# Kernel optimization log

Measured on AMD Instinct MI355X. Metric: run time of the kernel, lower is better.

## Reference

```python
import jax, jax.numpy as jnp
import numpy as np

N = 100000   # num nodes
D = 64       # in_channels == out_channels (forced by zeros_like(x) accumulator)
E = 400000   # edges per edge type
T = 5        # number of edge types (hardcoded list in the module)


def setup_inputs() -> dict:
    key = jax.random.key(0)
    k1, k2, k3, k4, k5 = jax.random.split(key, 5)
    x = jax.random.normal(k1, (N, D), dtype=jnp.float32)
    # 5 edge types, each [2, E] of node indices (row 0 = src, row 1 = dst)
    edges = jax.random.randint(k2, (T, 2, E), 0, N)
    # per-edge-type Linear(2D -> D): weight [2D, D] and bias [D]
    W = jax.random.normal(k3, (T, 2 * D, D), dtype=jnp.float32) * (1.0 / np.sqrt(2 * D))
    b = jax.random.normal(k4, (T, D), dtype=jnp.float32) * 0.01
    edge_attention = jax.random.normal(k5, (T,), dtype=jnp.float32)
    return {"x": x, "W": W, "b": b, "edge_attention": edge_attention, "edges": edges}


def reference(x, W, b, edge_attention, edges):
    # softmax over the 5 edge types (F.softmax(self.edge_attention, dim=0))
    weights = jax.nn.softmax(edge_attention)              # [T]
    src = edges[:, 0, :]                                  # [T, E]
    dst = edges[:, 1, :]                                  # [T, E]
    # gather: edge_features = cat([x[src], x[dst]], dim=1)
    feats = jnp.concatenate([x[src], x[dst]], axis=-1)    # [T, E, 2D]
    # per-edge-type MLP: Linear(2D->D) + ReLU
    proj = jax.nn.relu(jnp.einsum('tef,tfd->ted', feats, W) + b[:, None, :])  # [T, E, D]
    # scatter-add into src nodes, then mean via clamped bincount
    seg_sum = jax.vmap(lambda s, p: jax.ops.segment_sum(p, s, num_segments=N))(src, proj)  # [T, N, D]
    counts = jax.vmap(lambda s: jax.ops.segment_sum(jnp.ones(s.shape, jnp.float32), s, num_segments=N))(src)  # [T, N]
    counts = jnp.maximum(counts, 1.0)[:, :, None]         # clamp(min=1)
    node_proj = seg_sum / counts                          # [T, N, D]
    # attention-weighted sum across edge types
    return jnp.einsum('t,tnd->nd', weights, node_proj)    # [N, D]
```

## Files before the change

### kernel.cpp

```cpp
#include <hip/hip_runtime.h>
#include <hip/hip_bf16.h>

#define NN 100000
#define DD 64
#define EE 400000
#define TT 5

#define CH 40
#define BPC 2500
#define PSPLIT 32
#define PESL (EE / PSPLIT)
#define PBN (TT * CH * PSPLIT)
#define PB_IDX(t, c, s) ((((t) * CH + (c)) * PSPLIT) + (s))

typedef __bf16 bf16x8 __attribute__((ext_vector_type(8)));
typedef float  f32x4  __attribute__((ext_vector_type(4)));

#define OFF_XBF  0u
#define OFF_WT   12800000u
#define OFF_CTOT 12881920u
#define OFF_WGT  14881920u
#define OFF_PE   16886080u
#define OFF_PB   24886080u
#define OFF_DST  24914240u
#define OFF_SEG  32914240u

__device__ __forceinline__ unsigned short f2bf(float f) {
    union { float f; unsigned u; } v; v.f = f;
    unsigned u = v.u;
    return (unsigned short)((u + 0x7FFFu + ((u >> 16) & 1u)) >> 16);
}

__global__ __launch_bounds__(256) void k_init(
        const float* __restrict__ x, const float* __restrict__ W,
        const float* __restrict__ ea, const int* __restrict__ edges,
        unsigned short* __restrict__ xbf, unsigned short* __restrict__ wT,
        float* __restrict__ wgt, float* __restrict__ out,
        unsigned* __restrict__ pcnt) {
    int i = blockIdx.x * blockDim.x + threadIdx.x;
    if (i < NN * DD) {
        out[i] = 0.0f;
        xbf[i] = f2bf(x[i]);
    }
    if (i < TT * 128 * 64) {
        int t = i >> 13;
        int rem = i & 8191;
        int d = rem >> 7;
        int k = rem & 127;
        wT[i] = f2bf(W[t * 8192 + k * 64 + d]);
    }
    if (i == 0) {
        float m = -1e30f;
        for (int t = 0; t < TT; t++) m = fmaxf(m, ea[t]);
        float e[TT]; float s = 0.0f;
        for (int t = 0; t < TT; t++) { e[t] = __expf(ea[t] - m); s += e[t]; }
        for (int t = 0; t < TT; t++) wgt[t] = e[t] / s;
    }
    if (blockIdx.x < PSPLIT * TT) {
        const int s = blockIdx.x & (PSPLIT - 1);
        const int t = blockIdx.x >> 5;
        __shared__ unsigned h[CH];
        if (threadIdx.x < CH) h[threadIdx.x] = 0u;
        __syncthreads();
        const int4* srcp = reinterpret_cast<const int4*>(edges + (size_t)t * 2 * EE + s * PESL);
        for (int j = threadIdx.x; j < PESL / 4; j += 256) {
            int4 v = srcp[j];
            atomicAdd(&h[(unsigned)v.x / BPC], 1u);
            atomicAdd(&h[(unsigned)v.y / BPC], 1u);
            atomicAdd(&h[(unsigned)v.z / BPC], 1u);
            atomicAdd(&h[(unsigned)v.w / BPC], 1u);
        }
        __syncthreads();
        if (threadIdx.x < CH) pcnt[PB_IDX(t, threadIdx.x, s)] = h[threadIdx.x];
    }
}

__global__ __launch_bounds__(256) void k_pscat(const int* __restrict__ edges,
                                               const unsigned* __restrict__ pb,
                                               unsigned* __restrict__ pe) {
    const int s = blockIdx.x, t = blockIdx.y;
    const int tid = threadIdx.x;
    __shared__ unsigned pbs[PBN];
    __shared__ unsigned ssum[256];
    __shared__ unsigned lofs[CH];
    {
        const int base = tid * 25;
        unsigned v[25]; unsigned sum = 0u;
#pragma unroll
        for (int j = 0; j < 25; j++) { v[j] = pb[base + j]; sum += v[j]; }
        ssum[tid] = sum;
        __syncthreads();
        unsigned inc = sum;
        for (int d = 1; d < 256; d <<= 1) {
            unsigned a = (tid >= d) ? ssum[tid - d] : 0u;
            __syncthreads();
            inc += a;
            ssum[tid] = inc;
            __syncthreads();
        }
        unsigned run = inc - sum;
#pragma unroll
        for (int j = 0; j < 25; j++) { pbs[base + j] = run; run += v[j]; }
        __syncthreads();
        if (tid < CH) lofs[tid] = pbs[PB_IDX(t, tid, s)];
        __syncthreads();
    }
    const int* srcp = edges + (size_t)t * 2 * EE + s * PESL;
    const int* dstp = srcp + EE;
    for (int i = tid; i < PESL / 4; i += 256) {
        int4 v = reinterpret_cast<const int4*>(srcp)[i];
        int4 w = reinterpret_cast<const int4*>(dstp)[i];
        {
            unsigned c = (unsigned)v.x / BPC;
            unsigned o = atomicAdd(&lofs[c], 1u);
            pe[o] = (((unsigned)v.x - c * BPC) << 17) | (unsigned)w.x;
        }
        {
            unsigned c = (unsigned)v.y / BPC;
            unsigned o = atomicAdd(&lofs[c], 1u);
            pe[o] = (((unsigned)v.y - c * BPC) << 17) | (unsigned)w.y;
        }
        {
            unsigned c = (unsigned)v.z / BPC;
            unsigned o = atomicAdd(&lofs[c], 1u);
            pe[o] = (((unsigned)v.z - c * BPC) << 17) | (unsigned)w.z;
        }
        {
            unsigned c = (unsigned)v.w / BPC;
            unsigned o = atomicAdd(&lofs[c], 1u);
            pe[o] = (((unsigned)v.w - c * BPC) << 17) | (unsigned)w.w;
        }
    }
}

__global__ __launch_bounds__(512) void k_bsort(const unsigned* __restrict__ pe,
                                               const unsigned* __restrict__ pb,
                                               unsigned* __restrict__ cnt_tot,
                                               int* __restrict__ sdst,
                                               int* __restrict__ seg) {
    const int c = blockIdx.x, t = blockIdx.y;
    const int tid = threadIdx.x;
    __shared__ unsigned h[BPC];
    __shared__ unsigned curl[BPC];
    __shared__ unsigned ssum[512];
    __shared__ unsigned stsh[2];

    const int K = (t * CH + c) * PSPLIT;

    unsigned part = 0u;
    for (int i = tid; i < K; i += 512) part += pb[i];
    ssum[tid] = part;
    __syncthreads();
    for (int d = 256; d > 0; d >>= 1) {
        if (tid < d) ssum[tid] += ssum[tid + d];
        __syncthreads();
    }
    if (tid == 0) stsh[0] = ssum[0];
    unsigned part2 = (tid < PSPLIT) ? pb[K + tid] : 0u;
    __syncthreads();
    ssum[tid] = part2;
    __syncthreads();
    for (int d = 256; d > 0; d >>= 1) {
        if (tid < d) ssum[tid] += ssum[tid + d];
        __syncthreads();
    }
    if (tid == 0) stsh[1] = ssum[0];
    for (int i = tid; i < BPC; i += 512) h[i] = 0u;
    __syncthreads();
    const unsigned st = stsh[0];
    const unsigned en = st + stsh[1];

    for (unsigned i = st + tid; i < en; i += 512)
        atomicAdd(&h[pe[i] >> 17], 1u);
    __syncthreads();

    unsigned* outp = cnt_tot + t * NN + c * BPC;
    for (int i = tid; i < BPC; i += 512) outp[i] = h[i];

    {
        const int base = tid * 5;
        unsigned v[5]; unsigned sum = 0u;
#pragma unroll
        for (int j = 0; j < 5; j++) {
            int g = base + j;
            v[j] = (g < BPC) ? h[g] : 0u;
            sum += v[j];
        }
        ssum[tid] = sum;
        __syncthreads();
        unsigned inc = sum;
        for (int d = 1; d < 512; d <<= 1) {
            unsigned a = (tid >= d) ? ssum[tid - d] : 0u;
            __syncthreads();
            inc += a;
            ssum[tid] = inc;
            __syncthreads();
        }
        unsigned run = st + inc - sum;
#pragma unroll
        for (int j = 0; j < 5; j++) {
            int g = base + j;
            if (g < BPC) {
                curl[g] = run;
                const int node = c * BPC + g;
                for (unsigned jj = 0; jj < v[j]; jj++) seg[run + jj] = node;
                run += v[j];
            }
        }
    }
    __syncthreads();

    for (unsigned i = st + tid; i < en; i += 512) {
        unsigned p = pe[i];
        sdst[atomicAdd(&curl[p >> 17], 1u)] = (int)(p & 0x1FFFFu);
    }
}

__global__ __launch_bounds__(256) void k_edge(
    const unsigned short* __restrict__ xbf, const unsigned short* __restrict__ wT,
    const float* __restrict__ b, const int* __restrict__ sdst,
    const int* __restrict__ seg, const unsigned* __restrict__ cnt,
    const float* __restrict__ wgt, float* __restrict__ out) {
    const int t  = blockIdx.y;
    const int e0 = blockIdx.x * 128;

    __shared__ __align__(16) unsigned short Ab[128][136];
    __shared__ float scale_s[128];
    __shared__ int   src_s[132];

    const int tid = threadIdx.x;

    {
        int e = tid >> 1, half = tid & 1;
        size_t pos = (size_t)t * EE + e0 + e;
        int idx = half ? sdst[pos] : seg[pos];
        const float4* g = reinterpret_cast<const float4*>(xbf + (size_t)idx * 64);
        float4* l = reinterpret_cast<float4*>(&Ab[e][half * 64]);
#pragma unroll
        for (int c = 0; c < 8; c++) l[c] = g[c];
        if (half == 0) {
            src_s[e] = idx;
            scale_s[e] = wgt[t] / (float)cnt[t * NN + idx];
        }
    }
    __syncthreads();

    const int wv = tid >> 6, lane = tid & 63;
    const int m16 = lane & 15, quad = lane >> 4;
    const unsigned short* wrow = wT + (size_t)t * 8192;

    f32x4 acc[2][4];
#pragma unroll
    for (int tm = 0; tm < 2; tm++)
#pragma unroll
        for (int tn = 0; tn < 4; tn++)
            acc[tm][tn] = (f32x4){0.f, 0.f, 0.f, 0.f};

#pragma unroll
    for (int kk = 0; kk < 128; kk += 32) {
        const int kb = kk + quad * 8;
        bf16x8 af[2], bfr[4];
#pragma unroll
        for (int tm = 0; tm < 2; tm++)
            af[tm] = *reinterpret_cast<const bf16x8*>(&Ab[wv * 32 + tm * 16 + m16][kb]);
#pragma unroll
        for (int tn = 0; tn < 4; tn++)
            bfr[tn] = *reinterpret_cast<const bf16x8*>(wrow + (tn * 16 + m16) * 128 + kb);
#pragma unroll
        for (int tm = 0; tm < 2; tm++)
#pragma unroll
            for (int tn = 0; tn < 4; tn++)
                acc[tm][tn] = __builtin_amdgcn_mfma_f32_16x16x32_bf16(
                    af[tm], bfr[tn], acc[tm][tn], 0, 0, 0);
    }

    __syncthreads();

    float bias[4];
#pragma unroll
    for (int tn = 0; tn < 4; tn++) bias[tn] = b[t * 64 + tn * 16 + m16];

    float* proj = reinterpret_cast<float*>(&Ab[0][0]);
#pragma unroll
    for (int tm = 0; tm < 2; tm++) {
#pragma unroll
        for (int r = 0; r < 4; r++) {
            const int eloc = wv * 32 + tm * 16 + quad * 4 + r;
            const float s = scale_s[eloc];
#pragma unroll
            for (int tn = 0; tn < 4; tn++) {
                float v = acc[tm][tn][r] + bias[tn];
                v = v > 0.f ? v : 0.f;
                proj[eloc * 68 + tn * 16 + m16] = v * s;
            }
        }
    }

    {
        const int j0 = wv * 32;
        float sum = 0.f;
#pragma unroll
        for (int j = j0; j < j0 + 32; j++) {
            sum += proj[j * 68 + lane];
            const bool flush = (j == j0 + 31) || (src_s[j + 1] != src_s[j]);
            if (flush) {
                atomicAdd(out + (size_t)src_s[j] * 64 + lane, sum);
                sum = 0.f;
            }
        }
    }
}

extern "C" void kernel_launch(void* const* d_in, const int* in_sizes, int n_in,
                              void* d_out, int out_size, void* d_ws, size_t ws_size,
                              hipStream_t stream) {
    const float* x     = (const float*)d_in[0];
    const float* W     = (const float*)d_in[1];
    const float* b     = (const float*)d_in[2];
    const float* ea    = (const float*)d_in[3];
    const int*   edges = (const int*)d_in[4];
    float* out = (float*)d_out;

    char* ws = (char*)d_ws;
    unsigned short* xbf  = (unsigned short*)(ws + OFF_XBF);
    unsigned short* wT   = (unsigned short*)(ws + OFF_WT);
    unsigned* cnt_tot    = (unsigned*)(ws + OFF_CTOT);
    float* wgt           = (float*)(ws + OFF_WGT);
    unsigned* pe         = (unsigned*)(ws + OFF_PE);
    unsigned* pb         = (unsigned*)(ws + OFF_PB);
    int* sdst            = (int*)(ws + OFF_DST);
    int* seg             = (int*)(ws + OFF_SEG);

    k_init<<<(NN * DD) / 256, 256, 0, stream>>>(x, W, ea, edges, xbf, wT, wgt, out, pb);

    k_pscat<<<dim3(PSPLIT, TT), 256, 0, stream>>>(edges, pb, pe);

    k_bsort<<<dim3(CH, TT), 512, 0, stream>>>(pe, pb, cnt_tot, sdst, seg);

    dim3 grid(EE / 128, TT);
    k_edge<<<grid, 256, 0, stream>>>(xbf, wT, b, sdst, seg, cnt_tot, wgt, out);
}
```

Before: 317.4 us.

## Merge edge types into one global sort by source node, mask per-type GEMM

```diff
diff --git a/kernel.cpp b/kernel.cpp
--- a/kernel.cpp
+++ b/kernel.cpp
@@ -6,12 +6,14 @@
 #define EE 400000
 #define TT 5
 
-#define CH 40
-#define BPC 2500
+#define CH 160
+#define BPC 625
 #define PSPLIT 32
 #define PESL (EE / PSPLIT)
-#define PBN (TT * CH * PSPLIT)
-#define PB_IDX(t, c, s) ((((t) * CH + (c)) * PSPLIT) + (s))
+#define NSB (PSPLIT * TT)
+#define PBN (CH * NSB)
+#define NBIN (BPC * TT)
+#define NETOT (TT * EE)
 
 typedef __bf16 bf16x8 __attribute__((ext_vector_type(8)));
 typedef float  f32x4  __attribute__((ext_vector_type(4)));
@@ -20,8 +22,8 @@
 #define OFF_WT   12800000u
 #define OFF_CTOT 12881920u
 #define OFF_WGT  14881920u
+#define OFF_PB   14882048u
 #define OFF_PE   16886080u
-#define OFF_PB   24886080u
 #define OFF_DST  24914240u
 #define OFF_SEG  32914240u
 
@@ -56,9 +58,10 @@
         for (int t = 0; t < TT; t++) { e[t] = __expf(ea[t] - m); s += e[t]; }
         for (int t = 0; t < TT; t++) wgt[t] = e[t] / s;
     }
-    if (blockIdx.x < PSPLIT * TT) {
-        const int s = blockIdx.x & (PSPLIT - 1);
-        const int t = blockIdx.x >> 5;
+    if (blockIdx.x < NSB) {
+        const int sb = blockIdx.x;
+        const int s = sb & (PSPLIT - 1);
+        const int t = sb >> 5;
         __shared__ unsigned h[CH];
         if (threadIdx.x < CH) h[threadIdx.x] = 0u;
         __syncthreads();
@@ -71,64 +74,64 @@
             atomicAdd(&h[(unsigned)v.w / BPC], 1u);
         }
         __syncthreads();
-        if (threadIdx.x < CH) pcnt[PB_IDX(t, threadIdx.x, s)] = h[threadIdx.x];
-    }
+        if (threadIdx.x < CH) pcnt[threadIdx.x * NSB + sb] = h[threadIdx.x];
+    }
+}
+
+__global__ void k_pscan(unsigned* __restrict__ pb) {
+    __shared__ unsigned s[1024];
+    const int tid = threadIdx.x;
+    unsigned v[25]; unsigned sum = 0u;
+#pragma unroll
+    for (int j = 0; j < 25; j++) { v[j] = pb[tid * 25 + j]; sum += v[j]; }
+    s[tid] = sum;
+    __syncthreads();
+    unsigned inc = sum;
+    for (int d = 1; d < 1024; d <<= 1) {
+        unsigned a = (tid >= d) ? s[tid - d] : 0u;
+        __syncthreads();
+        inc += a;
+        s[tid] = inc;
+        __syncthreads();
+    }
+    unsigned run = inc - sum;
+#pragma unroll
+    for (int j = 0; j < 25; j++) { unsigned c = v[j]; pb[tid * 25 + j] = run; run += c; }
 }
 
 __global__ __launch_bounds__(256) void k_pscat(const int* __restrict__ edges,
-                                               const unsigned* __restrict__ pb,
+                                               const unsigned* __restrict__ pbase,
                                                unsigned* __restrict__ pe) {
     const int s = blockIdx.x, t = blockIdx.y;
-    const int tid = threadIdx.x;
-    __shared__ unsigned pbs[PBN];
-    __shared__ unsigned ssum[256];
+    const int sb = t * PSPLIT + s;
     __shared__ unsigned lofs[CH];
-    {
-        const int base = tid * 25;
-        unsigned v[25]; unsigned sum = 0u;
-#pragma unroll
-        for (int j = 0; j < 25; j++) { v[j] = pb[base + j]; sum += v[j]; }
-        ssum[tid] = sum;
-        __syncthreads();
-        unsigned inc = sum;
-        for (int d = 1; d < 256; d <<= 1) {
-            unsigned a = (tid >= d) ? ssum[tid - d] : 0u;
-            __syncthreads();
-            inc += a;
-            ssum[tid] = inc;
-            __syncthreads();
-        }
-        unsigned run = inc - sum;
-#pragma unroll
-        for (int j = 0; j < 25; j++) { pbs[base + j] = run; run += v[j]; }
-        __syncthreads();
-        if (tid < CH) lofs[tid] = pbs[PB_IDX(t, tid, s)];
-        __syncthreads();
-    }
+    if (threadIdx.x < CH) lofs[threadIdx.x] = pbase[threadIdx.x * NSB + sb];
+    __syncthreads();
     const int* srcp = edges + (size_t)t * 2 * EE + s * PESL;
     const int* dstp = srcp + EE;
-    for (int i = tid; i < PESL / 4; i += 256) {
+    const unsigned tb = (unsigned)t << 17;
+    for (int i = threadIdx.x; i < PESL / 4; i += 256) {
         int4 v = reinterpret_cast<const int4*>(srcp)[i];
         int4 w = reinterpret_cast<const int4*>(dstp)[i];
         {
             unsigned c = (unsigned)v.x / BPC;
             unsigned o = atomicAdd(&lofs[c], 1u);
-            pe[o] = (((unsigned)v.x - c * BPC) << 17) | (unsigned)w.x;
+            pe[o] = (((unsigned)v.x - c * BPC) << 20) | tb | (unsigned)w.x;
         }
         {
             unsigned c = (unsigned)v.y / BPC;
             unsigned o = atomicAdd(&lofs[c], 1u);
-            pe[o] = (((unsigned)v.y - c * BPC) << 17) | (unsigned)w.y;
+            pe[o] = (((unsigned)v.y - c * BPC) << 20) | tb | (unsigned)w.y;
         }
         {
             unsigned c = (unsigned)v.z / BPC;
             unsigned o = atomicAdd(&lofs[c], 1u);
-            pe[o] = (((unsigned)v.z - c * BPC) << 17) | (unsigned)w.z;
+            pe[o] = (((unsigned)v.z - c * BPC) << 20) | tb | (unsigned)w.z;
         }
         {
             unsigned c = (unsigned)v.w / BPC;
             unsigned o = atomicAdd(&lofs[c], 1u);
-            pe[o] = (((unsigned)v.w - c * BPC) << 17) | (unsigned)w.w;
+            pe[o] = (((unsigned)v.w - c * BPC) << 20) | tb | (unsigned)w.w;
         }
     }
 }
@@ -138,52 +141,36 @@
                                                unsigned* __restrict__ cnt_tot,
                                                int* __restrict__ sdst,
                                                int* __restrict__ seg) {
-    const int c = blockIdx.x, t = blockIdx.y;
+    const int c = blockIdx.x;
     const int tid = threadIdx.x;
-    __shared__ unsigned h[BPC];
-    __shared__ unsigned curl[BPC];
+    __shared__ unsigned h[NBIN];
+    __shared__ unsigned curl[NBIN];
     __shared__ unsigned ssum[512];
-    __shared__ unsigned stsh[2];
-
-    const int K = (t * CH + c) * PSPLIT;
-
-    unsigned part = 0u;
-    for (int i = tid; i < K; i += 512) part += pb[i];
-    ssum[tid] = part;
-    __syncthreads();
-    for (int d = 256; d > 0; d >>= 1) {
-        if (tid < d) ssum[tid] += ssum[tid + d];
-        __syncthreads();
-    }
-    if (tid == 0) stsh[0] = ssum[0];
-    unsigned part2 = (tid < PSPLIT) ? pb[K + tid] : 0u;
-    __syncthreads();
-    ssum[tid] = part2;
-    __syncthreads();
-    for (int d = 256; d > 0; d >>= 1) {
-        if (tid < d) ssum[tid] += ssum[tid + d];
-        __syncthreads();
-    }
-    if (tid == 0) stsh[1] = ssum[0];
-    for (int i = tid; i < BPC; i += 512) h[i] = 0u;
-    __syncthreads();
-    const unsigned st = stsh[0];
-    const unsigned en = st + stsh[1];
-
-    for (unsigned i = st + tid; i < en; i += 512)
-        atomicAdd(&h[pe[i] >> 17], 1u);
-    __syncthreads();
-
-    unsigned* outp = cnt_tot + t * NN + c * BPC;
-    for (int i = tid; i < BPC; i += 512) outp[i] = h[i];
+
+    const unsigned st = pb[c * NSB];
+    const unsigned en = (c == CH - 1) ? (unsigned)NETOT : pb[(c + 1) * NSB];
+
+    for (int i = tid; i < NBIN; i += 512) h[i] = 0u;
+    __syncthreads();
+
+    for (unsigned i = st + tid; i < en; i += 512) {
+        unsigned p = pe[i];
+        atomicAdd(&h[(p >> 20) * TT + ((p >> 17) & 7u)], 1u);
+    }
+    __syncthreads();
+
+    for (int g = tid; g < NBIN; g += 512) {
+        int sl = g / TT, t = g - sl * TT;
+        cnt_tot[t * NN + c * BPC + sl] = h[g];
+    }
 
     {
-        const int base = tid * 5;
-        unsigned v[5]; unsigned sum = 0u;
-#pragma unroll
-        for (int j = 0; j < 5; j++) {
+        const int base = tid * 7;
+        unsigned v[7]; unsigned sum = 0u;
+#pragma unroll
+        for (int j = 0; j < 7; j++) {
             int g = base + j;
-            v[j] = (g < BPC) ? h[g] : 0u;
+            v[j] = (g < NBIN) ? h[g] : 0u;
             sum += v[j];
         }
         ssum[tid] = sum;
@@ -198,12 +185,13 @@
         }
         unsigned run = st + inc - sum;
 #pragma unroll
-        for (int j = 0; j < 5; j++) {
+        for (int j = 0; j < 7; j++) {
             int g = base + j;
-            if (g < BPC) {
+            if (g < NBIN) {
                 curl[g] = run;
-                const int node = c * BPC + g;
-                for (unsigned jj = 0; jj < v[j]; jj++) seg[run + jj] = node;
+                int sl = g / TT, t = g - sl * TT;
+                int val = ((c * BPC + sl) << 3) | t;
+                for (unsigned jj = 0; jj < v[j]; jj++) seg[run + jj] = val;
                 run += v[j];
             }
         }
@@ -212,42 +200,54 @@
 
     for (unsigned i = st + tid; i < en; i += 512) {
         unsigned p = pe[i];
-        sdst[atomicAdd(&curl[p >> 17], 1u)] = (int)(p & 0x1FFFFu);
-    }
-}
-
-__global__ __launch_bounds__(256) void k_edge(
+        unsigned bin = (p >> 20) * TT + ((p >> 17) & 7u);
+        sdst[atomicAdd(&curl[bin], 1u)] = (int)(p & 0x1FFFFu);
+    }
+}
+
+__global__ __launch_bounds__(256) void k_edge7(
     const unsigned short* __restrict__ xbf, const unsigned short* __restrict__ wT,
     const float* __restrict__ b, const int* __restrict__ sdst,
     const int* __restrict__ seg, const unsigned* __restrict__ cnt,
     const float* __restrict__ wgt, float* __restrict__ out) {
-    const int t  = blockIdx.y;
     const int e0 = blockIdx.x * 128;
 
     __shared__ __align__(16) unsigned short Ab[128][136];
     __shared__ float scale_s[128];
     __shared__ int   src_s[132];
+    __shared__ int   t_s[132];
+    __shared__ float bs[TT * 64];
 
     const int tid = threadIdx.x;
 
     {
         int e = tid >> 1, half = tid & 1;
-        size_t pos = (size_t)t * EE + e0 + e;
-        int idx = half ? sdst[pos] : seg[pos];
+        int pos = e0 + e;
+        int sv = seg[pos];
+        int srcI = sv >> 3, tE = sv & 7;
+        int idx = half ? sdst[pos] : srcI;
         const float4* g = reinterpret_cast<const float4*>(xbf + (size_t)idx * 64);
         float4* l = reinterpret_cast<float4*>(&Ab[e][half * 64]);
 #pragma unroll
         for (int c = 0; c < 8; c++) l[c] = g[c];
         if (half == 0) {
-            src_s[e] = idx;
-            scale_s[e] = wgt[t] / (float)cnt[t * NN + idx];
-        }
-    }
+            src_s[e] = srcI;
+            t_s[e] = tE;
+            scale_s[e] = wgt[tE] / (float)cnt[tE * NN + srcI];
+        }
+    }
+    for (int i = tid; i < TT * 64; i += 256) bs[i] = b[i];
     __syncthreads();
 
     const int wv = tid >> 6, lane = tid & 63;
     const int m16 = lane & 15, quad = lane >> 4;
-    const unsigned short* wrow = wT + (size_t)t * 8192;
+
+    const int tA0 = t_s[wv * 32 + m16];
+    const int tA1 = t_s[wv * 32 + 16 + m16];
+
+    bf16x8 z;
+#pragma unroll
+    for (int i = 0; i < 8; i++) z[i] = (__bf16)0.0f;
 
     f32x4 acc[2][4];
 #pragma unroll
@@ -257,28 +257,29 @@
             acc[tm][tn] = (f32x4){0.f, 0.f, 0.f, 0.f};
 
 #pragma unroll
-    for (int kk = 0; kk < 128; kk += 32) {
-        const int kb = kk + quad * 8;
-        bf16x8 af[2], bfr[4];
-#pragma unroll
-        for (int tm = 0; tm < 2; tm++)
-            af[tm] = *reinterpret_cast<const bf16x8*>(&Ab[wv * 32 + tm * 16 + m16][kb]);
-#pragma unroll
-        for (int tn = 0; tn < 4; tn++)
-            bfr[tn] = *reinterpret_cast<const bf16x8*>(wrow + (tn * 16 + m16) * 128 + kb);
-#pragma unroll
-        for (int tm = 0; tm < 2; tm++)
+    for (int p = 0; p < TT; p++) {
+        const unsigned short* wrow = wT + (size_t)p * 8192;
+        const bool m0 = (tA0 == p), m1 = (tA1 == p);
+#pragma unroll
+        for (int kk = 0; kk < 128; kk += 32) {
+            const int kb = kk + quad * 8;
+            bf16x8 a0 = *reinterpret_cast<const bf16x8*>(&Ab[wv * 32 + m16][kb]);
+            bf16x8 a1 = *reinterpret_cast<const bf16x8*>(&Ab[wv * 32 + 16 + m16][kb]);
+            a0 = m0 ? a0 : z;
+            a1 = m1 ? a1 : z;
+            bf16x8 bfr[4];
 #pragma unroll
             for (int tn = 0; tn < 4; tn++)
-                acc[tm][tn] = __builtin_amdgcn_mfma_f32_16x16x32_bf16(
-                    af[tm], bfr[tn], acc[tm][tn], 0, 0, 0);
-    }
-
-    __syncthreads();
-
-    float bias[4];
-#pragma unroll
-    for (int tn = 0; tn < 4; tn++) bias[tn] = b[t * 64 + tn * 16 + m16];
+                bfr[tn] = *reinterpret_cast<const bf16x8*>(wrow + (tn * 16 + m16) * 128 + kb);
+#pragma unroll
+            for (int tn = 0; tn < 4; tn++) {
+                acc[0][tn] = __builtin_amdgcn_mfma_f32_16x16x32_bf16(a0, bfr[tn], acc[0][tn], 0, 0, 0);
+                acc[1][tn] = __builtin_amdgcn_mfma_f32_16x16x32_bf16(a1, bfr[tn], acc[1][tn], 0, 0, 0);
+            }
+        }
+    }
+
+    __syncthreads();
 
     float* proj = reinterpret_cast<float*>(&Ab[0][0]);
 #pragma unroll
@@ -287,9 +288,10 @@
         for (int r = 0; r < 4; r++) {
             const int eloc = wv * 32 + tm * 16 + quad * 4 + r;
             const float s = scale_s[eloc];
+            const int tE = t_s[eloc];
 #pragma unroll
             for (int tn = 0; tn < 4; tn++) {
-                float v = acc[tm][tn][r] + bias[tn];
+                float v = acc[tm][tn][r] + bs[tE * 64 + tn * 16 + m16];
                 v = v > 0.f ? v : 0.f;
                 proj[eloc * 68 + tn * 16 + m16] = v * s;
             }
@@ -333,10 +335,11 @@
 
     k_init<<<(NN * DD) / 256, 256, 0, stream>>>(x, W, ea, edges, xbf, wT, wgt, out, pb);
 
+    k_pscan<<<1, 1024, 0, stream>>>(pb);
+
     k_pscat<<<dim3(PSPLIT, TT), 256, 0, stream>>>(edges, pb, pe);
 
-    k_bsort<<<dim3(CH, TT), 512, 0, stream>>>(pe, pb, cnt_tot, sdst, seg);
-
-    dim3 grid(EE / 128, TT);
-    k_edge<<<grid, 256, 0, stream>>>(xbf, wT, b, sdst, seg, cnt_tot, wgt, out);
-}
+    k_bsort<<<CH, 512, 0, stream>>>(pe, pb, cnt_tot, sdst, seg);
+
+    k_edge7<<<NETOT / 128, 256, 0, stream>>>(xbf, wT, b, sdst, seg, cnt_tot, wgt, out);
+}
```

Measured after the change: 743.7 us. 2.34x slower.

## Use finer bucket partitioning with a global two-level prefix scan for edge sort

Applied to the files above, without the earlier changes.

```diff
diff --git a/kernel.cpp b/kernel.cpp
--- a/kernel.cpp
+++ b/kernel.cpp
@@ -6,12 +6,15 @@
 #define EE 400000
 #define TT 5
 
-#define CH 40
-#define BPC 2500
-#define PSPLIT 32
+#define CH 160
+#define BPC 625
+#define PSPLIT 100
 #define PESL (EE / PSPLIT)
+#define NSB (PSPLIT * TT)
 #define PBN (TT * CH * PSPLIT)
 #define PB_IDX(t, c, s) ((((t) * CH + (c)) * PSPLIT) + (s))
+#define PSA_B 80
+#define NETOT (TT * EE)
 
 typedef __bf16 bf16x8 __attribute__((ext_vector_type(8)));
 typedef float  f32x4  __attribute__((ext_vector_type(4)));
@@ -20,8 +23,9 @@
 #define OFF_WT   12800000u
 #define OFF_CTOT 12881920u
 #define OFF_WGT  14881920u
+#define OFF_PB   14882048u
+#define OFF_BS   15202304u
 #define OFF_PE   16886080u
-#define OFF_PB   24886080u
 #define OFF_DST  24914240u
 #define OFF_SEG  32914240u
 
@@ -56,9 +60,10 @@
         for (int t = 0; t < TT; t++) { e[t] = __expf(ea[t] - m); s += e[t]; }
         for (int t = 0; t < TT; t++) wgt[t] = e[t] / s;
     }
-    if (blockIdx.x < PSPLIT * TT) {
-        const int s = blockIdx.x & (PSPLIT - 1);
-        const int t = blockIdx.x >> 5;
+    if (blockIdx.x < NSB) {
+        const int sb = blockIdx.x;
+        const int t = sb / PSPLIT;
+        const int s = sb - t * PSPLIT;
         __shared__ unsigned h[CH];
         if (threadIdx.x < CH) h[threadIdx.x] = 0u;
         __syncthreads();
@@ -75,19 +80,117 @@
     }
 }
 
+__global__ void k_pscanA(unsigned* __restrict__ pb, unsigned* __restrict__ bsums) {
+    __shared__ unsigned s[1024];
+    const int tid = threadIdx.x;
+    const int g = blockIdx.x * 1024 + tid;
+    const unsigned v = (g < PBN) ? pb[g] : 0u;
+    s[tid] = v;
+    __syncthreads();
+    unsigned inc = v;
+    for (int d = 1; d < 1024; d <<= 1) {
+        unsigned a = (tid >= d) ? s[tid - d] : 0u;
+        __syncthreads();
+        inc += a;
+        s[tid] = inc;
+        __syncthreads();
+    }
+    if (g < PBN) pb[g] = inc - v;
+    if (tid == 1023) bsums[blockIdx.x] = inc;
+}
+
+__global__ void k_pscanB(unsigned* __restrict__ bsums) {
+    __shared__ unsigned s[PSA_B];
+    const int tid = threadIdx.x;
+    const unsigned v = (tid < PSA_B) ? bsums[tid] : 0u;
+    if (tid < PSA_B) s[tid] = v;
+    __syncthreads();
+    unsigned inc = v;
+    for (int d = 1; d < PSA_B; d <<= 1) {
+        unsigned a = (tid >= d && tid < PSA_B) ? s[tid - d] : 0u;
+        __syncthreads();
+        inc += a;
+        if (tid < PSA_B) s[tid] = inc;
+        __syncthreads();
+    }
+    if (tid < PSA_B) bsums[tid] = inc - v;
+}
+
 __global__ __launch_bounds__(256) void k_pscat(const int* __restrict__ edges,
                                                const unsigned* __restrict__ pb,
+                                               const unsigned* __restrict__ bsums,
                                                unsigned* __restrict__ pe) {
     const int s = blockIdx.x, t = blockIdx.y;
+    __shared__ unsigned lofs[CH];
+    if (threadIdx.x < CH) {
+        const int idx = PB_IDX(t, threadIdx.x, s);
+        lofs[threadIdx.x] = pb[idx] + bsums[idx >> 10];
+    }
+    __syncthreads();
+    const int* srcp = edges + (size_t)t * 2 * EE + s * PESL;
+    const int* dstp = srcp + EE;
+    for (int i = threadIdx.x; i < PESL / 4; i += 256) {
+        int4 v = reinterpret_cast<const int4*>(srcp)[i];
+        int4 w = reinterpret_cast<const int4*>(dstp)[i];
+        {
+            unsigned c = (unsigned)v.x / BPC;
+            unsigned o = atomicAdd(&lofs[c], 1u);
+            pe[o] = (((unsigned)v.x - c * BPC) << 17) | (unsigned)w.x;
+        }
+        {
+            unsigned c = (unsigned)v.y / BPC;
+            unsigned o = atomicAdd(&lofs[c], 1u);
+            pe[o] = (((unsigned)v.y - c * BPC) << 17) | (unsigned)w.y;
+        }
+        {
+            unsigned c = (unsigned)v.z / BPC;
+            unsigned o = atomicAdd(&lofs[c], 1u);
+            pe[o] = (((unsigned)v.z - c * BPC) << 17) | (unsigned)w.z;
+        }
+        {
+            unsigned c = (unsigned)v.w / BPC;
+            unsigned o = atomicAdd(&lofs[c], 1u);
+            pe[o] = (((unsigned)v.w - c * BPC) << 17) | (unsigned)w.w;
+        }
+    }
+}
+
+__global__ __launch_bounds__(256) void k_bsort(const unsigned* __restrict__ pe,
+                                               const unsigned* __restrict__ pb,
+                                               const unsigned* __restrict__ bsums,
+                                               unsigned* __restrict__ cnt_tot,
+                                               int* __restrict__ sdst,
+                                               int* __restrict__ seg) {
+    const int c = blockIdx.x, t = blockIdx.y;
     const int tid = threadIdx.x;
-    __shared__ unsigned pbs[PBN];
+    __shared__ unsigned h[BPC];
+    __shared__ unsigned curl[BPC];
     __shared__ unsigned ssum[256];
-    __shared__ unsigned lofs[CH];
+
+    const int K = (t * CH + c) * PSPLIT;
+    const unsigned st = pb[K] + bsums[K >> 10];
+    const int K2 = K + PSPLIT;
+    const unsigned en = (K2 >= PBN) ? (unsigned)NETOT : (pb[K2] + bsums[K2 >> 10]);
+
+    for (int i = tid; i < BPC; i += 256) h[i] = 0u;
+    __syncthreads();
+
+    for (unsigned i = st + tid; i < en; i += 256)
+        atomicAdd(&h[pe[i] >> 17], 1u);
+    __syncthreads();
+
+    unsigned* outp = cnt_tot + t * NN + c * BPC;
+    for (int i = tid; i < BPC; i += 256) outp[i] = h[i];
+
     {
-        const int base = tid * 25;
-        unsigned v[25]; unsigned sum = 0u;
-#pragma unroll
-        for (int j = 0; j < 25; j++) { v[j] = pb[base + j]; sum += v[j]; }
+        const int base = tid * 3;
+        unsigned v[3]; unsigned sum = 0u;
+#pragma unroll
+        for (int j = 0; j < 3; j++) {
+            int g = base + j;
+            v[j] = (g < BPC) ? h[g] : 0u;
+            sum += v[j];
+        }
         ssum[tid] = sum;
         __syncthreads();
         unsigned inc = sum;
@@ -98,107 +201,9 @@
             ssum[tid] = inc;
             __syncthreads();
         }
-        unsigned run = inc - sum;
-#pragma unroll
-        for (int j = 0; j < 25; j++) { pbs[base + j] = run; run += v[j]; }
-        __syncthreads();
-        if (tid < CH) lofs[tid] = pbs[PB_IDX(t, tid, s)];
-        __syncthreads();
-    }
-    const int* srcp = edges + (size_t)t * 2 * EE + s * PESL;
-    const int* dstp = srcp + EE;
-    for (int i = tid; i < PESL / 4; i += 256) {
-        int4 v = reinterpret_cast<const int4*>(srcp)[i];
-        int4 w = reinterpret_cast<const int4*>(dstp)[i];
-        {
-            unsigned c = (unsigned)v.x / BPC;
-            unsigned o = atomicAdd(&lofs[c], 1u);
-            pe[o] = (((unsigned)v.x - c * BPC) << 17) | (unsigned)w.x;
-        }
-        {
-            unsigned c = (unsigned)v.y / BPC;
-            unsigned o = atomicAdd(&lofs[c], 1u);
-            pe[o] = (((unsigned)v.y - c * BPC) << 17) | (unsigned)w.y;
-        }
-        {
-            unsigned c = (unsigned)v.z / BPC;
-            unsigned o = atomicAdd(&lofs[c], 1u);
-            pe[o] = (((unsigned)v.z - c * BPC) << 17) | (unsigned)w.z;
-        }
-        {
-            unsigned c = (unsigned)v.w / BPC;
-            unsigned o = atomicAdd(&lofs[c], 1u);
-            pe[o] = (((unsigned)v.w - c * BPC) << 17) | (unsigned)w.w;
-        }
-    }
-}
-
-__global__ __launch_bounds__(512) void k_bsort(const unsigned* __restrict__ pe,
-                                               const unsigned* __restrict__ pb,
-                                               unsigned* __restrict__ cnt_tot,
-                                               int* __restrict__ sdst,
-                                               int* __restrict__ seg) {
-    const int c = blockIdx.x, t = blockIdx.y;
-    const int tid = threadIdx.x;
-    __shared__ unsigned h[BPC];
-    __shared__ unsigned curl[BPC];
-    __shared__ unsigned ssum[512];
-    __shared__ unsigned stsh[2];
-
-    const int K = (t * CH + c) * PSPLIT;
-
-    unsigned part = 0u;
-    for (int i = tid; i < K; i += 512) part += pb[i];
-    ssum[tid] = part;
-    __syncthreads();
-    for (int d = 256; d > 0; d >>= 1) {
-        if (tid < d) ssum[tid] += ssum[tid + d];
-        __syncthreads();
-    }
-    if (tid == 0) stsh[0] = ssum[0];
-    unsigned part2 = (tid < PSPLIT) ? pb[K + tid] : 0u;
-    __syncthreads();
-    ssum[tid] = part2;
-    __syncthreads();
-    for (int d = 256; d > 0; d >>= 1) {
-        if (tid < d) ssum[tid] += ssum[tid + d];
-        __syncthreads();
-    }
-    if (tid == 0) stsh[1] = ssum[0];
-    for (int i = tid; i < BPC; i += 512) h[i] = 0u;
-    __syncthreads();
-    const unsigned st = stsh[0];
-    const unsigned en = st + stsh[1];
-
-    for (unsigned i = st + tid; i < en; i += 512)
-        atomicAdd(&h[pe[i] >> 17], 1u);
-    __syncthreads();
-
-    unsigned* outp = cnt_tot + t * NN + c * BPC;
-    for (int i = tid; i < BPC; i += 512) outp[i] = h[i];
-
-    {
-        const int base = tid * 5;
-        unsigned v[5]; unsigned sum = 0u;
-#pragma unroll
-        for (int j = 0; j < 5; j++) {
-            int g = base + j;
-            v[j] = (g < BPC) ? h[g] : 0u;
-            sum += v[j];
-        }
-        ssum[tid] = sum;
-        __syncthreads();
-        unsigned inc = sum;
-        for (int d = 1; d < 512; d <<= 1) {
-            unsigned a = (tid >= d) ? ssum[tid - d] : 0u;
-            __syncthreads();
-            inc += a;
-            ssum[tid] = inc;
-            __syncthreads();
-        }
         unsigned run = st + inc - sum;
 #pragma unroll
-        for (int j = 0; j < 5; j++) {
+        for (int j = 0; j < 3; j++) {
             int g = base + j;
             if (g < BPC) {
                 curl[g] = run;
@@ -210,7 +215,7 @@
     }
     __syncthreads();
 
-    for (unsigned i = st + tid; i < en; i += 512) {
+    for (unsigned i = st + tid; i < en; i += 256) {
         unsigned p = pe[i];
         sdst[atomicAdd(&curl[p >> 17], 1u)] = (int)(p & 0x1FFFFu);
     }
@@ -326,16 +331,20 @@
     unsigned short* wT   = (unsigned short*)(ws + OFF_WT);
     unsigned* cnt_tot    = (unsigned*)(ws + OFF_CTOT);
     float* wgt           = (float*)(ws + OFF_WGT);
+    unsigned* pb         = (unsigned*)(ws + OFF_PB);
+    unsigned* bsums      = (unsigned*)(ws + OFF_BS);
     unsigned* pe         = (unsigned*)(ws + OFF_PE);
-    unsigned* pb         = (unsigned*)(ws + OFF_PB);
     int* sdst            = (int*)(ws + OFF_DST);
     int* seg             = (int*)(ws + OFF_SEG);
 
     k_init<<<(NN * DD) / 256, 256, 0, stream>>>(x, W, ea, edges, xbf, wT, wgt, out, pb);
 
-    k_pscat<<<dim3(PSPLIT, TT), 256, 0, stream>>>(edges, pb, pe);
-
-    k_bsort<<<dim3(CH, TT), 512, 0, stream>>>(pe, pb, cnt_tot, sdst, seg);
+    k_pscanA<<<PSA_B, 1024, 0, stream>>>(pb, bsums);
+    k_pscanB<<<1, 128, 0, stream>>>(bsums);
+
+    k_pscat<<<dim3(PSPLIT, TT), 256, 0, stream>>>(edges, pb, bsums, pe);
+
+    k_bsort<<<dim3(CH, TT), 256, 0, stream>>>(pe, pb, bsums, cnt_tot, sdst, seg);
 
     dim3 grid(EE / 128, TT);
     k_edge<<<grid, 256, 0, stream>>>(xbf, wT, b, sdst, seg, cnt_tot, wgt, out);
```

Result: no change. 311.5 us (-1.9%).
